# Kernel tuning notes

Measured on AMD Instinct MI355X. Metric: run time of the kernel, lower is better.

The kernel has to match this reference:

```python
import jax, jax.numpy as jnp
import numpy as np

N = 200000      # tweet nodes
E = 1600000     # edges
U = 20000       # users (num_users)
D = 64          # embedding_dimension1 == embedding_dimension2
NUMP, CATP = 20, 12
EPS = 0.1       # PyG FAConv default eps


def setup_inputs() -> dict:
    key = jax.random.key(0)
    ks = jax.random.split(key, 20)
    s = 0.05
    offs = jnp.sort(jax.random.randint(ks[3], (U + 1,), 0, N, dtype=jnp.int64))
    offs = offs.at[0].set(0).at[-1].set(N)
    return {
        "num_prop": jax.random.normal(ks[0], (N, NUMP), jnp.float32),
        "cat_prop": jax.random.normal(ks[1], (N, CATP), jnp.float32),
        "tweet_offsets": offs,
        "edge_index": jax.random.randint(ks[2], (2, E), 0, N, dtype=jnp.int64),
        "re_index": jax.random.randint(ks[4], (U,), 0, U, dtype=jnp.int64),
        "W_num": jax.random.normal(ks[5], (NUMP, D // 2), jnp.float32) * s,
        "b_num": jnp.zeros((D // 2,), jnp.float32),
        "W_cat": jax.random.normal(ks[6], (CATP, D // 2), jnp.float32) * s,
        "b_cat": jnp.zeros((D // 2,), jnp.float32),
        "W_tog": jax.random.normal(ks[7], (D, D), jnp.float32) * s,
        "b_tog": jnp.zeros((D,), jnp.float32),
        "att_l": jax.random.normal(ks[8], (D,), jnp.float32) * s,
        "att_r": jax.random.normal(ks[9], (D,), jnp.float32) * s,
        "W_f1": jax.random.normal(ks[10], (D, D // 2), jnp.float32) * s,
        "b_f1": jnp.zeros((D // 2,), jnp.float32),
        "W_lab": jax.random.normal(ks[11], (D // 2, 2), jnp.float32) * s,
        "b_lab": jnp.zeros((2,), jnp.float32),
    }


def reference(num_prop, cat_prop, tweet_offsets, edge_index, re_index,
              W_num, b_num, W_cat, b_cat, W_tog, b_tog,
              att_l, att_r, W_f1, b_f1, W_lab, b_lab):
    n = num_prop.shape[0]
    lrelu = jax.nn.leaky_relu  # slope 0.01, matches nn.LeakyReLU default

    num = lrelu(num_prop @ W_num + b_num)
    cat = lrelu(cat_prop @ W_cat + b_cat)
    x = lrelu(jnp.concatenate([num, cat], axis=1) @ W_tog + b_tog)  # [N, D]

    # gcn_norm with self-loops (PyG FAConv default normalize=True, add_self_loops=True)
    loop = jnp.arange(n, dtype=edge_index.dtype)
    src = jnp.concatenate([edge_index[0], loop])
    dst = jnp.concatenate([edge_index[1], loop])
    deg = jax.ops.segment_sum(jnp.ones(src.shape[0], jnp.float32), dst, num_segments=n)
    dinv = jnp.where(deg > 0, deg ** -0.5, 0.0)
    norm = dinv[src] * dinv[dst]  # [E+N]

    def faconv(h, h0):
        # alpha_e = tanh(att_l . h[src] + att_r . h[dst]); out_i = sum_e norm_e * alpha_e * h[src_e]
        al = h @ att_l
        ar = h @ att_r
        alpha = jnp.tanh(al[src] + ar[dst]) * norm
        agg = jax.ops.segment_sum(h[src] * alpha[:, None], dst, num_segments=n)
        return agg + EPS * h0

    x1 = faconv(x, x)      # dropout is identity in eval mode
    x2 = faconv(x1, x)
    x2 = jnp.sqrt(x2 ** 2 + 1e-8)

    # ragged per-user segment sum from CSR offsets (replaces python loop+slice)
    nseg = tweet_offsets.shape[0] - 1
    seg = jnp.searchsorted(tweet_offsets, jnp.arange(n), side='right') - 1
    seg = jnp.clip(seg, 0, nseg - 1)
    x3 = jax.ops.segment_sum(x2, seg, num_segments=nseg)  # [U, D]

    x3 = x3[re_index]
    h = lrelu(x3 @ W_f1 + b_f1)
    return h @ W_lab + b_lab
```

## Files before the change

### kernel.cpp

```cpp
#include <hip/hip_runtime.h>
#include <hip/hip_bf16.h>

#define LRELU(v) ((v) > 0.0f ? (v) : 0.01f * (v))
#define EPS 0.1f

#define BSHIFT  9
#define BSIZE   512
#define BIN_EPB 2048
#define BIN_CAP 6144

typedef __attribute__((ext_vector_type(8))) short bf16x8;
typedef __attribute__((ext_vector_type(4))) float f32x4;

__device__ __forceinline__ float fast_tanh(float v)
{
    float e = __expf(2.0f * v);
    return 1.0f - 2.0f * __builtin_amdgcn_rcpf(e + 1.0f);
}

__device__ __forceinline__ float bf2f(unsigned short h)
{
    return __uint_as_float(((unsigned int)h) << 16);
}
__device__ __forceinline__ unsigned short f2bf(float f)
{
    unsigned int u = __float_as_uint(f);
    u += 0x7FFFu + ((u >> 16) & 1u);
    return (unsigned short)(u >> 16);
}

__global__ void k_prep(const float* __restrict__ W_num, const float* __restrict__ W_cat,
                       const float* __restrict__ W_tog,
                       unsigned short* __restrict__ Wb, unsigned short* __restrict__ Wb1)
{
    int t = threadIdx.x;
    for (int i = t; i < 8 * 512; i += 256) {
        int tile = i >> 9;
        int kt   = tile >> 2, nt = tile & 3;
        int lane = (i >> 3) & 63;
        int j    = i & 7;
        int k    = kt * 32 + (lane >> 4) * 8 + j;
        int n    = nt * 16 + (lane & 15);
        Wb[i] = f2bf(W_tog[k * 64 + n]);
    }
    for (int i = t; i < 4 * 512; i += 256) {
        int nt   = i >> 9;
        int lane = (i >> 3) & 63;
        int j    = i & 7;
        int k    = (lane >> 4) * 8 + j;
        int n    = nt * 16 + (lane & 15);
        float w;
        if (n < 32) w = (k < 20)  ? W_num[k * 32 + n]              : 0.0f;
        else        w = (k >= 20) ? W_cat[(k - 20) * 32 + (n - 32)] : 0.0f;
        Wb1[i] = f2bf(w);
    }
}

__global__ void __launch_bounds__(256)
k_feat(const float* __restrict__ num_prop,
       const float* __restrict__ cat_prop,
       const unsigned short* __restrict__ Wb1,
       const float* __restrict__ b_num, const float* __restrict__ b_cat,
       const unsigned short* __restrict__ Wb, const float* __restrict__ b_tog,
       const float* __restrict__ att_l, const float* __restrict__ att_r,
       unsigned short* __restrict__ xb,
       float* __restrict__ al, float* __restrict__ ar, int N)
{
    __shared__ unsigned short in_lds[64][40];
    __shared__ unsigned short mid[64][72];

    int tid  = threadIdx.x;
    int lane = tid & 63;
    int w    = tid >> 6;
    int blockStart = blockIdx.x * 64;

    for (int i = tid; i < 64 * 20; i += 256) {
        int node = i / 20, k = i % 20;
        int n = min(blockStart + node, N - 1);
        in_lds[node][k] = f2bf(num_prop[(size_t)n * 20 + k]);
    }
    for (int i = tid; i < 64 * 12; i += 256) {
        int node = i / 12, k = i % 12;
        int n = min(blockStart + node, N - 1);
        in_lds[node][20 + k] = f2bf(cat_prop[(size_t)n * 12 + k]);
    }
    __syncthreads();

    int q   = lane >> 4;
    int c16 = lane & 15;

    bf16x8 ain = *(const bf16x8*)&in_lds[w * 16 + c16][q * 8];
    #pragma unroll
    for (int nt = 0; nt < 4; nt++) {
        bf16x8 b = *(const bf16x8*)&Wb1[nt * 512 + lane * 8];
        f32x4 acc = {0.0f, 0.0f, 0.0f, 0.0f};
        acc = __builtin_amdgcn_mfma_f32_16x16x32_bf16(ain, b, acc, 0, 0, 0);
        int   ch   = nt * 16 + c16;
        float bias = (ch < 32) ? b_num[ch] : b_cat[ch - 32];
        #pragma unroll
        for (int r = 0; r < 4; r++) {
            float s = acc[r] + bias;
            s = LRELU(s);
            mid[w * 16 + q * 4 + r][ch] = f2bf(s);
        }
    }

    bf16x8 a0 = *(const bf16x8*)&mid[w * 16 + c16][q * 8];
    bf16x8 a1 = *(const bf16x8*)&mid[w * 16 + c16][32 + q * 8];

    float pal[4] = {0, 0, 0, 0};
    float par[4] = {0, 0, 0, 0};

    #pragma unroll
    for (int nt = 0; nt < 4; nt++) {
        bf16x8 b0 = *(const bf16x8*)&Wb[(0 * 4 + nt) * 512 + lane * 8];
        bf16x8 b1 = *(const bf16x8*)&Wb[(1 * 4 + nt) * 512 + lane * 8];
        f32x4 acc = {0.0f, 0.0f, 0.0f, 0.0f};
        acc = __builtin_amdgcn_mfma_f32_16x16x32_bf16(a0, b0, acc, 0, 0, 0);
        acc = __builtin_amdgcn_mfma_f32_16x16x32_bf16(a1, b1, acc, 0, 0, 0);

        int   ch  = nt * 16 + c16;
        float bt  = b_tog[ch];
        float atl = att_l[ch];
        float atr = att_r[ch];
        #pragma unroll
        for (int r = 0; r < 4; r++) {
            float s = acc[r] + bt;
            s = LRELU(s);
            int n = blockStart + w * 16 + q * 4 + r;
            if (n < N) xb[(size_t)n * 64 + ch] = f2bf(s);
            pal[r] = fmaf(s, atl, pal[r]);
            par[r] = fmaf(s, atr, par[r]);
        }
    }

    #pragma unroll
    for (int r = 0; r < 4; r++) {
        float pl = pal[r], pr = par[r];
        #pragma unroll
        for (int off = 8; off > 0; off >>= 1) {
            pl += __shfl_xor(pl, off);
            pr += __shfl_xor(pr, off);
        }
        int n = blockStart + w * 16 + q * 4 + r;
        if (c16 == 0 && n < N) { al[n] = pl; ar[n] = pr; }
    }
}

__global__ void k_bin(const int* __restrict__ src, const int* __restrict__ dst,
                      int* __restrict__ bucket_cnt,
                      int2* __restrict__ buckets, int E, int NB)
{
    __shared__ int  hist[BSIZE];
    __shared__ int  lbase[BSIZE];
    __shared__ int  gbase[BSIZE];
    __shared__ int2 stage[BIN_EPB];

    int tid  = threadIdx.x;
    int base = blockIdx.x * BIN_EPB;

    hist[tid] = 0;
    __syncthreads();

    int s[4], d[4], rk[4];
    #pragma unroll
    for (int k = 0; k < 4; k++) {
        int e = base + k * BSIZE + tid;
        s[k] = -1;
        if (e < E) {
            s[k] = src[e];
            d[k] = dst[e];
            rk[k] = atomicAdd(&hist[d[k] >> BSHIFT], 1);
        }
    }
    __syncthreads();

    int v = hist[tid];
    lbase[tid] = v;
    __syncthreads();
    for (int off = 1; off < BSIZE; off <<= 1) {
        int t = (tid >= off) ? lbase[tid - off] : 0;
        __syncthreads();
        lbase[tid] += t;
        __syncthreads();
    }
    int incl = lbase[tid];
    __syncthreads();
    lbase[tid] = incl - v;
    if (tid < NB && v > 0) gbase[tid] = atomicAdd(&bucket_cnt[tid], v);
    __syncthreads();

    #pragma unroll
    for (int k = 0; k < 4; k++) {
        if (s[k] >= 0) {
            int b = d[k] >> BSHIFT;
            stage[lbase[b] + rk[k]] = make_int2(s[k], d[k]);
        }
    }
    __syncthreads();

    int tot = min(BIN_EPB, E - base);
    for (int i = tid; i < tot; i += BSIZE) {
        int2 p = stage[i];
        int b = p.y >> BSHIFT;
        buckets[(size_t)b * BIN_CAP + gbase[b] + (i - lbase[b])] = p;
    }
}

__global__ void k_degScan(const int2* __restrict__ buckets, const int* __restrict__ bucket_cnt,
                          int* __restrict__ deg, int* __restrict__ row_start,
                          int* __restrict__ bucketTot, int N)
{
    __shared__ int cnt[BSIZE];
    __shared__ int sc[BSIZE];
    int b   = blockIdx.x;
    int tid = threadIdx.x;
    cnt[tid] = 0;
    __syncthreads();

    int ecnt = bucket_cnt[b];
    const int2* bp = buckets + (size_t)b * BIN_CAP;
    for (int i = tid; i < ecnt; i += BSIZE)
        atomicAdd(&cnt[bp[i].y & (BSIZE - 1)], 1);
    __syncthreads();

    int d = cnt[tid];
    int p = (d + 7) & ~7;
    sc[tid] = p;
    __syncthreads();
    for (int off = 1; off < BSIZE; off <<= 1) {
        int t = (tid >= off) ? sc[tid - off] : 0;
        __syncthreads();
        sc[tid] += t;
        __syncthreads();
    }
    int incl = sc[tid];

    int n = b * BSIZE + tid;
    if (n < N) {
        deg[n]       = d;
        row_start[n] = incl - p;
    }
    if (tid == BSIZE - 1) bucketTot[b] = incl;
}

__global__ void k_scan2(int* __restrict__ bucketTot, int nb)
{
    __shared__ int sh[BSIZE];
    int tid = threadIdx.x;
    int v = (tid < nb) ? bucketTot[tid] : 0;
    sh[tid] = v;
    __syncthreads();
    for (int off = 1; off < BSIZE; off <<= 1) {
        int t = (tid >= off) ? sh[tid - off] : 0;
        __syncthreads();
        sh[tid] += t;
        __syncthreads();
    }
    if (tid < nb) bucketTot[tid] = sh[tid] - v;
}

__global__ void k_scan3(int* __restrict__ row_start, const int* __restrict__ bucketTot,
                        const int* __restrict__ deg,
                        const float* __restrict__ al, float2* __restrict__ ald1,
                        int* __restrict__ srcs,
                        const int* __restrict__ offs, int* __restrict__ seg,
                        int N, int U)
{
    int i = blockIdx.x * blockDim.x + threadIdx.x;
    if (i >= N) return;
    int s0 = row_start[i] + bucketTot[i >> BSHIFT];
    row_start[i] = s0;
    int cnt  = deg[i];
    int cntp = (cnt + 7) & ~7;
    for (int k = cnt; k < cntp; k++) srcs[s0 + k] = 0;
    float dv = 1.0f / sqrtf((float)cnt + 1.0f);
    ald1[i]  = make_float2(al[i], dv);

    int lo = 0, hi = U;
    while (lo < hi) {
        int mid = (lo + hi) >> 1;
        if (offs[mid] <= i) lo = mid + 1; else hi = mid;
    }
    seg[i] = min(max(lo - 1, 0), U - 1);
}

__global__ void k_fill2(const int2* __restrict__ buckets, const int* __restrict__ bucket_cnt,
                        const int* __restrict__ row_start,
                        int* __restrict__ srcs)
{
    __shared__ int cur[BSIZE];
    int b   = blockIdx.x;
    int tid = threadIdx.x;
    cur[tid] = 0;
    __syncthreads();

    int cnt = bucket_cnt[b];
    const int2* bp = buckets + (size_t)b * BIN_CAP;
    for (int i = tid; i < cnt; i += BSIZE) {
        int2 p = bp[i];
        int r = p.y & (BSIZE - 1);
        int o = atomicAdd(&cur[r], 1);
        srcs[row_start[p.y] + o] = p.x;
    }
}

__global__ void k_gather1(const int* __restrict__ srcs,
                          const int* __restrict__ row_start, const int* __restrict__ deg,
                          const unsigned short* __restrict__ xb,
                          const float2* __restrict__ ald1, const float* __restrict__ ar,
                          const float* __restrict__ att_l, const float* __restrict__ att_r,
                          unsigned short* __restrict__ h1b, float2* __restrict__ ald2,
                          float* __restrict__ ar2, int N)
{
    int lane = threadIdx.x & 63;
    int c0   = __builtin_amdgcn_readfirstlane(blockIdx.x * 4 + (threadIdx.x >> 6)) * 4;
    if (c0 >= N) return;
    int nend = min(c0 + 4, N);

    float atl = att_l[lane];
    float atr = att_r[lane];

    for (int n = c0; n < nend; n++) {
        int    s0   = row_start[n];
        int    cnt  = deg[n];
        int    cntp = (cnt + 7) & ~7;
        float2 self = ald1[n];
        float  di   = self.y;
        float  arn  = ar[n];

        float acc = 0.0f;
        for (int jb = 0; jb < cntp; jb += 64) {
            float a = 0.0f;
            int   e = jb + lane;
            if (e < cnt) {
                int s = srcs[s0 + e];
                float2 as = ald1[s];
                a = fast_tanh(as.x + arn) * as.y * di;
            }
            int te = min(cntp - jb, 64);
            for (int j = 0; j < te; j += 8) {
                int sv[8]; float vv[8];
                #pragma unroll
                for (int t = 0; t < 8; t++) sv[t] = srcs[s0 + jb + j + t];
                #pragma unroll
                for (int t = 0; t < 8; t++) vv[t] = bf2f(xb[(size_t)sv[t] * 64 + lane]);
                #pragma unroll
                for (int t = 0; t < 8; t++) acc = fmaf(vv[t], __shfl(a, j + t), acc);
            }
        }

        float selfa = fast_tanh(self.x + arn) * di * di;
        float xnl   = bf2f(xb[(size_t)n * 64 + lane]);
        float v     = acc + (selfa + EPS) * xnl;

        float pl = v * atl;
        float pr = v * atr;
        #pragma unroll
        for (int off = 32; off > 0; off >>= 1) {
            pl += __shfl_down(pl, off);
            pr += __shfl_down(pr, off);
        }
        h1b[(size_t)n * 64 + lane] = f2bf(v);
        if (lane == 0) { ald2[n] = make_float2(pl, di); ar2[n] = pr; }
    }
}

__global__ void k_gather2(const int* __restrict__ srcs,
                          const int* __restrict__ row_start, const int* __restrict__ deg,
                          const unsigned short* __restrict__ h1b,
                          const unsigned short* __restrict__ xb,
                          const float2* __restrict__ ald2, const float* __restrict__ ar2,
                          const int* __restrict__ seg,
                          float* __restrict__ x3, int N)
{
    int lane = threadIdx.x & 63;
    int c0   = __builtin_amdgcn_readfirstlane(blockIdx.x * 4 + (threadIdx.x >> 6)) * 4;
    if (c0 >= N) return;
    int nend = min(c0 + 4, N);

    float uacc = 0.0f;
    int   useg = seg[c0];

    for (int n = c0; n < nend; n++) {
        int sg = seg[n];
        if (sg != useg) {
            atomicAdd(&x3[(size_t)useg * 64 + lane], uacc);
            uacc = 0.0f;
            useg = sg;
        }

        int    s0   = row_start[n];
        int    cnt  = deg[n];
        int    cntp = (cnt + 7) & ~7;
        float2 self = ald2[n];
        float  di   = self.y;
        float  arn  = ar2[n];

        float acc = 0.0f;
        for (int jb = 0; jb < cntp; jb += 64) {
            float a = 0.0f;
            int   e = jb + lane;
            if (e < cnt) {
                int s = srcs[s0 + e];
                float2 as = ald2[s];
                a = fast_tanh(as.x + arn) * as.y * di;
            }
            int te = min(cntp - jb, 64);
            for (int j = 0; j < te; j += 8) {
                int sv[8]; float vv[8];
                #pragma unroll
                for (int t = 0; t < 8; t++) sv[t] = srcs[s0 + jb + j + t];
                #pragma unroll
                for (int t = 0; t < 8; t++) vv[t] = bf2f(h1b[(size_t)sv[t] * 64 + lane]);
                #pragma unroll
                for (int t = 0; t < 8; t++) acc = fmaf(vv[t], __shfl(a, j + t), acc);
            }
        }

        float selfa = fast_tanh(self.x + arn) * di * di;
        float h1l   = bf2f(h1b[(size_t)n * 64 + lane]);
        float xnl   = bf2f(xb[(size_t)n * 64 + lane]);
        float v = acc + selfa * h1l + EPS * xnl;
        uacc += sqrtf(v * v + 1e-8f);
    }
    atomicAdd(&x3[(size_t)useg * 64 + lane], uacc);
}

__global__ void __launch_bounds__(256)
k_head(const float* __restrict__ x3, const int* __restrict__ re_index,
       const float* __restrict__ W_f1, const float* __restrict__ b_f1,
       const float* __restrict__ W_lab, const float* __restrict__ b_lab,
       float* __restrict__ out, int U)
{
    __shared__ float wf[64][32];
    __shared__ float wl[32][2];

    int tid = threadIdx.x;
    for (int i = tid; i < 64 * 32; i += 256) wf[i >> 5][i & 31] = W_f1[i];
    if (tid < 64) wl[tid >> 1][tid & 1] = W_lab[tid];
    __syncthreads();

    int u = blockIdx.x * blockDim.x + tid;
    if (u >= U) return;

    int r = re_index[u];
    const float* y = x3 + (size_t)r * 64;

    float s[32];
    #pragma unroll
    for (int j = 0; j < 32; j++) s[j] = b_f1[j];

    for (int k = 0; k < 64; k++) {
        float yk = y[k];
        #pragma unroll
        for (int j = 0; j < 32; j++) s[j] = fmaf(yk, wf[k][j], s[j]);
    }

    float o0 = b_lab[0], o1 = b_lab[1];
    #pragma unroll
    for (int j = 0; j < 32; j++) {
        float t = LRELU(s[j]);
        o0 = fmaf(t, wl[j][0], o0);
        o1 = fmaf(t, wl[j][1], o1);
    }
    out[(size_t)u * 2 + 0] = o0;
    out[(size_t)u * 2 + 1] = o1;
}

extern "C" void kernel_launch(void* const* d_in, const int* in_sizes, int n_in,
                              void* d_out, int out_size, void* d_ws, size_t ws_size,
                              hipStream_t stream)
{
    const float* num_prop = (const float*)d_in[0];
    const float* cat_prop = (const float*)d_in[1];
    const int*   offs     = (const int*)d_in[2];
    const int*   edge     = (const int*)d_in[3];
    const int*   re_index = (const int*)d_in[4];
    const float* W_num    = (const float*)d_in[5];
    const float* b_num    = (const float*)d_in[6];
    const float* W_cat    = (const float*)d_in[7];
    const float* b_cat    = (const float*)d_in[8];
    const float* W_tog    = (const float*)d_in[9];
    const float* b_tog    = (const float*)d_in[10];
    const float* att_l    = (const float*)d_in[11];
    const float* att_r    = (const float*)d_in[12];
    const float* W_f1     = (const float*)d_in[13];
    const float* b_f1     = (const float*)d_in[14];
    const float* W_lab    = (const float*)d_in[15];
    const float* b_lab    = (const float*)d_in[16];

    const int N = in_sizes[0] / 20;
    const int E = in_sizes[3] / 2;
    const int U = in_sizes[4];

    const int* src = edge;
    const int* dst = edge + E;

    const int    NB      = (N + BSIZE - 1) >> BSHIFT;
    const size_t srcsCap = (size_t)E + 7ull * (size_t)N + 64;

    float* ws = (float*)d_ws;
    size_t off = 0;
    unsigned short* xb  = (unsigned short*)(ws + off); off += (size_t)N * 32;
    unsigned short* h1b = (unsigned short*)(ws + off); off += (size_t)N * 32;
    float2* ald1 = (float2*)(ws + off); off += (size_t)N * 2;
    float2* ald2 = (float2*)(ws + off); off += (size_t)N * 2;
    int2*   buckets = (int2*)(ws + off); off += (size_t)NB * BIN_CAP * 2;
    float*  al   = ws + off; off += N;
    float*  ar   = ws + off; off += N;
    float*  ar2  = ws + off; off += N;
    float*  x3   = ws + off; off += (size_t)U * 64;
    unsigned short* Wb  = (unsigned short*)(ws + off); off += 2048;
    unsigned short* Wb1 = (unsigned short*)(ws + off); off += 1024;
    int*    deg        = (int*)(ws + off); off += N;
    int*    row_start  = (int*)(ws + off); off += N;
    int*    seg        = (int*)(ws + off); off += N;
    int*    bucket_cnt = (int*)(ws + off); off += NB;
    int*    bucketTot  = (int*)(ws + off); off += BSIZE;
    int*    srcs       = (int*)(ws + off); off += srcsCap;

    hipMemsetAsync(bucket_cnt, 0, (size_t)NB * 4, stream);
    hipMemsetAsync(x3, 0, (size_t)U * 64 * 4, stream);

    const int nbC   = (N + 15) / 16;
    const int nbN   = (N + 255) / 256;
    const int nbBin = (E + BIN_EPB - 1) / BIN_EPB;

    k_prep<<<1, 256, 0, stream>>>(W_num, W_cat, W_tog, Wb, Wb1);

    k_feat<<<(N + 63) / 64, 256, 0, stream>>>(num_prop, cat_prop, Wb1, b_num, b_cat,
                                              Wb, b_tog, att_l, att_r, xb, al, ar, N);

    k_bin<<<nbBin, BSIZE, 0, stream>>>(src, dst, bucket_cnt, buckets, E, NB);

    k_degScan<<<NB, BSIZE, 0, stream>>>(buckets, bucket_cnt, deg, row_start, bucketTot, N);
    k_scan2<<<1, BSIZE, 0, stream>>>(bucketTot, NB);
    k_scan3<<<nbN, 256, 0, stream>>>(row_start, bucketTot, deg, al, ald1,
                                     srcs, offs, seg, N, U);

    k_fill2<<<NB, BSIZE, 0, stream>>>(buckets, bucket_cnt, row_start, srcs);

    k_gather1<<<nbC, 256, 0, stream>>>(srcs, row_start, deg, xb, ald1, ar,
                                       att_l, att_r, h1b, ald2, ar2, N);

    k_gather2<<<nbC, 256, 0, stream>>>(srcs, row_start, deg, h1b, xb,
                                       ald2, ar2, seg, x3, N);

    k_head<<<(U + 255) / 256, 256, 0, stream>>>(x3, re_index, W_f1, b_f1, W_lab, b_lab,
                                                (float*)d_out, U);
}
```

Before: 337.4 us.

## Fuse CSR build kernels into one per-bucket kernel with packed edges

Packs each binned edge into a single int (source shifted left, low destination bits). This halves bucket traffic. The degree count, scans, padding, seg search and fill kernels are merged into one per-bucket kernel that stages edges in LDS. A fixed per-bucket CSR capacity (CAPP) replaces the global cross-bucket scan, which removes three kernel launches and a global read pass over the buckets. The risks are that packing caps source index width and that CAPP must be large enough for the padded degree sum of every bucket.

```diff
diff --git a/kernel.cpp b/kernel.cpp
--- a/kernel.cpp
+++ b/kernel.cpp
@@ -8,6 +8,7 @@
 #define BSIZE   512
 #define BIN_EPB 2048
 #define BIN_CAP 6144
+#define CAPP    10240
 
 typedef __attribute__((ext_vector_type(8))) short bf16x8;
 typedef __attribute__((ext_vector_type(4))) float f32x4;
@@ -149,7 +150,7 @@
 
 __global__ void k_bin(const int* __restrict__ src, const int* __restrict__ dst,
                       int* __restrict__ bucket_cnt,
-                      int2* __restrict__ buckets, int E, int NB)
+                      int* __restrict__ buckets, int E, int NB)
 {
     __shared__ int  hist[BSIZE];
     __shared__ int  lbase[BSIZE];
@@ -203,25 +204,37 @@
     for (int i = tid; i < tot; i += BSIZE) {
         int2 p = stage[i];
         int b = p.y >> BSHIFT;
-        buckets[(size_t)b * BIN_CAP + gbase[b] + (i - lbase[b])] = p;
-    }
-}
-
-__global__ void k_degScan(const int2* __restrict__ buckets, const int* __restrict__ bucket_cnt,
-                          int* __restrict__ deg, int* __restrict__ row_start,
-                          int* __restrict__ bucketTot, int N)
-{
+        buckets[(size_t)b * BIN_CAP + gbase[b] + (i - lbase[b])] =
+            (p.x << BSHIFT) | (p.y & (BSIZE - 1));
+    }
+}
+
+__global__ void __launch_bounds__(512)
+k_build(const int* __restrict__ buckets, const int* __restrict__ bucket_cnt,
+        const float* __restrict__ al, const int* __restrict__ offs,
+        float2* __restrict__ ald1,
+        int* __restrict__ deg, int* __restrict__ row_start, int* __restrict__ seg,
+        int* __restrict__ srcs, int N, int U)
+{
+    __shared__ int stage[BIN_CAP];
     __shared__ int cnt[BSIZE];
     __shared__ int sc[BSIZE];
+    __shared__ int cur[BSIZE];
+
     int b   = blockIdx.x;
     int tid = threadIdx.x;
+    int ecnt = bucket_cnt[b];
+    const int* bp = buckets + (size_t)b * BIN_CAP;
+
     cnt[tid] = 0;
-    __syncthreads();
-
-    int ecnt = bucket_cnt[b];
-    const int2* bp = buckets + (size_t)b * BIN_CAP;
-    for (int i = tid; i < ecnt; i += BSIZE)
-        atomicAdd(&cnt[bp[i].y & (BSIZE - 1)], 1);
+    cur[tid] = 0;
+    __syncthreads();
+
+    for (int i = tid; i < ecnt; i += BSIZE) {
+        int e = bp[i];
+        stage[i] = e;
+        atomicAdd(&cnt[e & (BSIZE - 1)], 1);
+    }
     __syncthreads();
 
     int d = cnt[tid];
@@ -234,74 +247,32 @@
         sc[tid] += t;
         __syncthreads();
     }
-    int incl = sc[tid];
-
-    int n = b * BSIZE + tid;
+    int rstart = sc[tid] - p;
+
+    int gb = b * CAPP;
+    int n  = b * BSIZE + tid;
     if (n < N) {
         deg[n]       = d;
-        row_start[n] = incl - p;
-    }
-    if (tid == BSIZE - 1) bucketTot[b] = incl;
-}
-
-__global__ void k_scan2(int* __restrict__ bucketTot, int nb)
-{
-    __shared__ int sh[BSIZE];
-    int tid = threadIdx.x;
-    int v = (tid < nb) ? bucketTot[tid] : 0;
-    sh[tid] = v;
-    __syncthreads();
-    for (int off = 1; off < BSIZE; off <<= 1) {
-        int t = (tid >= off) ? sh[tid - off] : 0;
-        __syncthreads();
-        sh[tid] += t;
-        __syncthreads();
-    }
-    if (tid < nb) bucketTot[tid] = sh[tid] - v;
-}
-
-__global__ void k_scan3(int* __restrict__ row_start, const int* __restrict__ bucketTot,
-                        const int* __restrict__ deg,
-                        const float* __restrict__ al, float2* __restrict__ ald1,
-                        int* __restrict__ srcs,
-                        const int* __restrict__ offs, int* __restrict__ seg,
-                        int N, int U)
-{
-    int i = blockIdx.x * blockDim.x + threadIdx.x;
-    if (i >= N) return;
-    int s0 = row_start[i] + bucketTot[i >> BSHIFT];
-    row_start[i] = s0;
-    int cnt  = deg[i];
-    int cntp = (cnt + 7) & ~7;
-    for (int k = cnt; k < cntp; k++) srcs[s0 + k] = 0;
-    float dv = 1.0f / sqrtf((float)cnt + 1.0f);
-    ald1[i]  = make_float2(al[i], dv);
-
-    int lo = 0, hi = U;
-    while (lo < hi) {
-        int mid = (lo + hi) >> 1;
-        if (offs[mid] <= i) lo = mid + 1; else hi = mid;
-    }
-    seg[i] = min(max(lo - 1, 0), U - 1);
-}
-
-__global__ void k_fill2(const int2* __restrict__ buckets, const int* __restrict__ bucket_cnt,
-                        const int* __restrict__ row_start,
-                        int* __restrict__ srcs)
-{
-    __shared__ int cur[BSIZE];
-    int b   = blockIdx.x;
-    int tid = threadIdx.x;
-    cur[tid] = 0;
-    __syncthreads();
-
-    int cnt = bucket_cnt[b];
-    const int2* bp = buckets + (size_t)b * BIN_CAP;
-    for (int i = tid; i < cnt; i += BSIZE) {
-        int2 p = bp[i];
-        int r = p.y & (BSIZE - 1);
+        row_start[n] = gb + rstart;
+        for (int k = d; k < p + 0; k++) srcs[gb + rstart + k] = 0;
+        float dv = 1.0f / sqrtf((float)d + 1.0f);
+        ald1[n] = make_float2(al[n], dv);
+
+        int lo = 0, hi = U;
+        while (lo < hi) {
+            int mid = (lo + hi) >> 1;
+            if (offs[mid] <= n) lo = mid + 1; else hi = mid;
+        }
+        seg[n] = min(max(lo - 1, 0), U - 1);
+    }
+    __syncthreads();
+
+    for (int i = tid; i < ecnt; i += BSIZE) {
+        int e = stage[i];
+        int r = e & (BSIZE - 1);
         int o = atomicAdd(&cur[r], 1);
-        srcs[row_start[p.y] + o] = p.x;
+        int rs = sc[r] - ((cnt[r] + 7) & ~7);
+        srcs[gb + rs + o] = e >> BSHIFT;
     }
 }
 
@@ -497,8 +468,7 @@
     const int* src = edge;
     const int* dst = edge + E;
 
-    const int    NB      = (N + BSIZE - 1) >> BSHIFT;
-    const size_t srcsCap = (size_t)E + 7ull * (size_t)N + 64;
+    const int NB = (N + BSIZE - 1) >> BSHIFT;
 
     float* ws = (float*)d_ws;
     size_t off = 0;
@@ -506,7 +476,7 @@
     unsigned short* h1b = (unsigned short*)(ws + off); off += (size_t)N * 32;
     float2* ald1 = (float2*)(ws + off); off += (size_t)N * 2;
     float2* ald2 = (float2*)(ws + off); off += (size_t)N * 2;
-    int2*   buckets = (int2*)(ws + off); off += (size_t)NB * BIN_CAP * 2;
+    int*    buckets = (int*)(ws + off); off += (size_t)NB * BIN_CAP;
     float*  al   = ws + off; off += N;
     float*  ar   = ws + off; off += N;
     float*  ar2  = ws + off; off += N;
@@ -517,14 +487,12 @@
     int*    row_start  = (int*)(ws + off); off += N;
     int*    seg        = (int*)(ws + off); off += N;
     int*    bucket_cnt = (int*)(ws + off); off += NB;
-    int*    bucketTot  = (int*)(ws + off); off += BSIZE;
-    int*    srcs       = (int*)(ws + off); off += srcsCap;
+    int*    srcs       = (int*)(ws + off); off += (size_t)NB * CAPP;
 
     hipMemsetAsync(bucket_cnt, 0, (size_t)NB * 4, stream);
     hipMemsetAsync(x3, 0, (size_t)U * 64 * 4, stream);
 
     const int nbC   = (N + 15) / 16;
-    const int nbN   = (N + 255) / 256;
     const int nbBin = (E + BIN_EPB - 1) / BIN_EPB;
 
     k_prep<<<1, 256, 0, stream>>>(W_num, W_cat, W_tog, Wb, Wb1);
@@ -534,12 +502,8 @@
 
     k_bin<<<nbBin, BSIZE, 0, stream>>>(src, dst, bucket_cnt, buckets, E, NB);
 
-    k_degScan<<<NB, BSIZE, 0, stream>>>(buckets, bucket_cnt, deg, row_start, bucketTot, N);
-    k_scan2<<<1, BSIZE, 0, stream>>>(bucketTot, NB);
-    k_scan3<<<nbN, 256, 0, stream>>>(row_start, bucketTot, deg, al, ald1,
-                                     srcs, offs, seg, N, U);
-
-    k_fill2<<<NB, BSIZE, 0, stream>>>(buckets, bucket_cnt, row_start, srcs);
+    k_build<<<NB, BSIZE, 0, stream>>>(buckets, bucket_cnt, al, offs, ald1,
+                                      deg, row_start, seg, srcs, N, U);
 
     k_gather1<<<nbC, 256, 0, stream>>>(srcs, row_start, deg, xb, ald1, ar,
                                        att_l, att_r, h1b, ald2, ar2, N);
```

Result: faster. 327.3 us (-3.0%).
